# Performance work log

Hardware: AMD Instinct MI355X
Metric: run time of the kernel (lower is better)

## Reference

```python
import jax, jax.numpy as jnp
import numpy as np

TEMPERATURE = 0.07
NORMALIZE = True
NEG_INF = -1e30


def setup_inputs() -> dict:
    key = jax.random.key(0)
    features = jax.random.normal(key, (8192, 512), dtype=jnp.float32)
    return {"features": features}


def reference(features):
    # features: [B, D]
    B = features.shape[0]
    if NORMALIZE:
        norm = jnp.linalg.norm(features, axis=1, keepdims=True)
        features = features / jnp.maximum(norm, 1e-12)
    # [B, B] similarity matrix
    sim = jnp.matmul(features, features.T) / TEMPERATURE

    # default SimCLR labels: arange(B//2) repeated twice -> pair (i, i + B//2)
    half = jnp.arange(B // 2, dtype=jnp.int32)
    labels = jnp.concatenate([half, half])
    eq = labels[None, :] == labels[:, None]          # [B, B]
    diag = jnp.eye(B, dtype=bool)
    mask_pos = eq & ~diag                            # positives per row

    # Original per-row CE: logits = cat(pos_sims, neg_sims) (= all j != i),
    # target index 0 = FIRST positive (lowest column index). Loss_i =
    # logsumexp_{j != i}(sim[i, j]) - sim[i, first_pos_i].
    sim_masked = jnp.where(diag, NEG_INF, sim)
    lse = jax.scipy.special.logsumexp(sim_masked, axis=1)   # [B]

    first_pos = jnp.argmax(mask_pos, axis=1)                 # first True per row
    pos_sim = jnp.take_along_axis(sim, first_pos[:, None], axis=1)[:, 0]

    has_pos = jnp.any(mask_pos, axis=1)
    losses = jnp.where(has_pos, lse - pos_sim, 0.0)
    count = jnp.maximum(jnp.sum(has_pos.astype(jnp.float32)), 1.0)
    return jnp.sum(losses) / count
```

## Files before the change

### kernel.cpp

```cpp
#include <hip/hip_runtime.h>
#include <hip/hip_bf16.h>
#include <stdint.h>

#define BATCH 8192
#define DIM   512
#define TILE  128
#define BK    64
#define NT    (BATCH / TILE)
#define NPAIR (NT * (NT + 1) / 2)
#define NXCD  8

#define FEAT_SCALE 4.5398164f
#define LN2        0.69314718055994531f

typedef __attribute__((ext_vector_type(8))) short short8;
typedef __attribute__((ext_vector_type(4))) float f32x4;

__device__ __forceinline__ void gld_lds16(const void* g, void* l) {
  __builtin_amdgcn_global_load_lds(
      (__attribute__((address_space(1))) void*)(uintptr_t)g,
      (__attribute__((address_space(3))) void*)(uintptr_t)l,
      16, 0, 0);
}

__global__ __launch_bounds__(256) void normalize_bf16(
    const float* __restrict__ x, __hip_bfloat16* __restrict__ o,
    float* __restrict__ rowsum) {
  const int wv = threadIdx.x >> 6, lane = threadIdx.x & 63;
  const int row = blockIdx.x * 4 + wv;
  if (lane == 0) rowsum[row] = 0.0f;
  const float4* xr = (const float4*)(x + (size_t)row * DIM);
  const float4 v0 = xr[lane];
  const float4 v1 = xr[lane + 64];
  float ss = v0.x * v0.x + v0.y * v0.y + v0.z * v0.z + v0.w * v0.w +
             v1.x * v1.x + v1.y * v1.y + v1.z * v1.z + v1.w * v1.w;
#pragma unroll
  for (int m = 32; m > 0; m >>= 1) ss += __shfl_xor(ss, m, 64);
  const float inv = FEAT_SCALE / fmaxf(sqrtf(ss), 1e-12f);
  ushort4 p0, p1;
  p0.x = __bfloat16_as_ushort(__float2bfloat16(v0.x * inv));
  p0.y = __bfloat16_as_ushort(__float2bfloat16(v0.y * inv));
  p0.z = __bfloat16_as_ushort(__float2bfloat16(v0.z * inv));
  p0.w = __bfloat16_as_ushort(__float2bfloat16(v0.w * inv));
  p1.x = __bfloat16_as_ushort(__float2bfloat16(v1.x * inv));
  p1.y = __bfloat16_as_ushort(__float2bfloat16(v1.y * inv));
  p1.z = __bfloat16_as_ushort(__float2bfloat16(v1.z * inv));
  p1.w = __bfloat16_as_ushort(__float2bfloat16(v1.w * inv));
  ushort4* orow = (ushort4*)(o + (size_t)row * DIM);
  orow[lane]      = p0;
  orow[lane + 64] = p1;
}

__global__ __launch_bounds__(256, 4) void sim_lse_kernel(
    const __hip_bfloat16* __restrict__ F, float* __restrict__ rowsum,
    float* __restrict__ possim) {
  __shared__ __hip_bfloat16 smem[2 * TILE * BK];
  __shared__ float rowAcc[TILE];
  __shared__ float colAcc[TILE];

  const int t = (blockIdx.x % NXCD) * (NPAIR / NXCD) + blockIdx.x / NXCD;

  int by = (int)((129.0f - sqrtf(129.0f * 129.0f - 8.0f * (float)t)) * 0.5f);
  if (by > NT - 1) by = NT - 1;
  if (by < 0) by = 0;
  while ((by + 1) * (129 - (by + 1)) / 2 <= t) ++by;
  while (by * (129 - by) / 2 > t) --by;
  const int bx = by + (t - by * (129 - by) / 2);
  const bool diagTile = (bx == by);

  const int rowBase = by * TILE;
  const int colBase = bx * TILE;

  const int tid   = threadIdx.x;
  const int lane  = tid & 63;
  const int wv    = tid >> 6;
  const int waveM = wv >> 1;
  const int waveN = wv & 1;
  const int quad  = lane >> 4;
  const int l15   = lane & 15;

  if (tid < TILE) { rowAcc[tid] = 0.0f; colAcc[tid] = 0.0f; }

  f32x4 acc[4][4] = {};

  const int sb = lane & 7;
  const __hip_bfloat16* gA[4];
  const __hip_bfloat16* gB[4];
  char* ldsA[4];
  char* ldsB[4];
#pragma unroll
  for (int c = 0; c < 4; ++c) {
    const int sRow = wv * 32 + c * 8 + (lane >> 3);
    const int g = sb ^ (sRow & 7);
    gA[c] = F + (size_t)(rowBase + sRow) * DIM + g * 8;
    gB[c] = F + (size_t)(colBase + sRow) * DIM + g * 8;
    ldsA[c] = (char*)smem + (wv * 4 + c) * 1024;
    ldsB[c] = (char*)smem + 16384 + (wv * 4 + c) * 1024;
  }

  int aOff[4], bOff[4];
#pragma unroll
  for (int i = 0; i < 4; ++i) {
    const int Ra = waveM * 64 + i * 16 + l15;
    aOff[i] = Ra * 128 + (quad ^ (Ra & 7)) * 16;
    const int Rb = waveN * 64 + i * 16 + l15;
    bOff[i] = 16384 + Rb * 128 + (quad ^ (Rb & 7)) * 16;
  }
  char* sbase = (char*)smem;

  for (int k0 = 0; k0 < DIM; k0 += BK) {
#pragma unroll
    for (int c = 0; c < 4; ++c) {
      gld_lds16(gA[c] + k0, ldsA[c]);
      gld_lds16(gB[c] + k0, ldsB[c]);
    }
    __syncthreads();

    short8 a[4], b[4];
#pragma unroll
    for (int i = 0; i < 4; ++i) {
      a[i] = *(const short8*)(sbase + aOff[i]);
      b[i] = *(const short8*)(sbase + bOff[i]);
    }
#pragma unroll
    for (int mi = 0; mi < 4; ++mi)
#pragma unroll
      for (int ni = 0; ni < 4; ++ni)
        acc[mi][ni] =
            __builtin_amdgcn_mfma_f32_16x16x32_bf16(a[mi], b[ni], acc[mi][ni], 0, 0, 0);
#pragma unroll
    for (int i = 0; i < 4; ++i) {
      a[i] = *(const short8*)(sbase + (aOff[i] ^ 64));
      b[i] = *(const short8*)(sbase + (bOff[i] ^ 64));
    }
#pragma unroll
    for (int mi = 0; mi < 4; ++mi)
#pragma unroll
      for (int ni = 0; ni < 4; ++ni)
        acc[mi][ni] =
            __builtin_amdgcn_mfma_f32_16x16x32_bf16(a[mi], b[ni], acc[mi][ni], 0, 0, 0);
    __syncthreads();
  }

  if (diagTile) {
#pragma unroll
    for (int mi = 0; mi < 4; ++mi) {
#pragma unroll
      for (int r = 0; r < 4; ++r) {
        const int lrow = waveM * 64 + mi * 16 + quad * 4 + r;
        float rsum = 0.0f;
#pragma unroll
        for (int ni = 0; ni < 4; ++ni) {
          const int lcol = waveN * 64 + ni * 16 + l15;
          rsum += (lcol == lrow) ? 0.0f : exp2f(acc[mi][ni][r]);
        }
#pragma unroll
        for (int m = 1; m < 16; m <<= 1) rsum += __shfl_xor(rsum, m, 64);
        if (l15 == 0) atomicAdd(&rowAcc[lrow], rsum);
      }
    }
  } else {
    const bool hasPos = (bx == by + 32);
    float colpart[4] = {0.0f, 0.0f, 0.0f, 0.0f};
#pragma unroll
    for (int mi = 0; mi < 4; ++mi) {
#pragma unroll
      for (int r = 0; r < 4; ++r) {
        const int lrow = waveM * 64 + mi * 16 + quad * 4 + r;
        float rsum = 0.0f;
#pragma unroll
        for (int ni = 0; ni < 4; ++ni) {
          const float s = acc[mi][ni][r];
          const float e = exp2f(s);
          rsum += e;
          colpart[ni] += e;
          if (hasPos) {
            const int lcol = waveN * 64 + ni * 16 + l15;
            if (lcol == lrow) {
              const int gi = rowBase + lrow;
              possim[gi] = s;
              possim[gi + 4096] = s;
            }
          }
        }
#pragma unroll
        for (int m = 1; m < 16; m <<= 1) rsum += __shfl_xor(rsum, m, 64);
        if (l15 == 0) atomicAdd(&rowAcc[lrow], rsum);
      }
    }
#pragma unroll
    for (int ni = 0; ni < 4; ++ni) {
      float c = colpart[ni];
      c += __shfl_xor(c, 16, 64);
      c += __shfl_xor(c, 32, 64);
      if (quad == 0) atomicAdd(&colAcc[waveN * 64 + ni * 16 + l15], c);
    }
  }
  __syncthreads();
  if (tid < TILE) {
    atomicAdd(&rowsum[rowBase + tid], rowAcc[tid]);
    if (!diagTile) atomicAdd(&rowsum[colBase + tid], colAcc[tid]);
  }
}

__global__ __launch_bounds__(1024) void finalize_kernel(
    const float* __restrict__ rowsum, const float* __restrict__ possim,
    float* __restrict__ out) {
  float acc = 0.0f;
  for (int i = threadIdx.x; i < BATCH; i += 1024)
    acc += __logf(rowsum[i]) - possim[i] * LN2;
#pragma unroll
  for (int m = 32; m > 0; m >>= 1) acc += __shfl_xor(acc, m, 64);
  __shared__ float ws[16];
  const int lane = threadIdx.x & 63, wv = threadIdx.x >> 6;
  if (lane == 0) ws[wv] = acc;
  __syncthreads();
  if (threadIdx.x == 0) {
    float tot = 0.0f;
#pragma unroll
    for (int k = 0; k < 16; ++k) tot += ws[k];
    out[0] = tot * (1.0f / (float)BATCH);
  }
}

extern "C" void kernel_launch(void* const* d_in, const int* in_sizes, int n_in,
                              void* d_out, int out_size, void* d_ws, size_t ws_size,
                              hipStream_t stream) {
  const float* x = (const float*)d_in[0];
  float* out = (float*)d_out;

  __hip_bfloat16* Fb = (__hip_bfloat16*)d_ws;
  float* rowsum = (float*)((char*)d_ws + (size_t)BATCH * DIM * sizeof(__hip_bfloat16));
  float* possim = rowsum + BATCH;

  normalize_bf16<<<BATCH / 4, 256, 0, stream>>>(x, Fb, rowsum);
  sim_lse_kernel<<<NPAIR, 256, 0, stream>>>(Fb, rowsum, possim);
  finalize_kernel<<<1, 1024, 0, stream>>>(rowsum, possim, out);
}
```

Baseline: 130.0 us.

## Replace shuffle+LDS-atomic row reduction with padded LDS transpose; drop XCD swizzle

```diff
diff --git a/kernel.cpp b/kernel.cpp
--- a/kernel.cpp
+++ b/kernel.cpp
@@ -8,7 +8,6 @@
 #define BK    64
 #define NT    (BATCH / TILE)
 #define NPAIR (NT * (NT + 1) / 2)
-#define NXCD  8
 
 #define FEAT_SCALE 4.5398164f
 #define LN2        0.69314718055994531f
@@ -55,11 +54,9 @@
     const __hip_bfloat16* __restrict__ F, float* __restrict__ rowsum,
     float* __restrict__ possim) {
   __shared__ __hip_bfloat16 smem[2 * TILE * BK];
-  __shared__ float rowAcc[TILE];
   __shared__ float colAcc[TILE];
 
-  const int t = (blockIdx.x % NXCD) * (NPAIR / NXCD) + blockIdx.x / NXCD;
-
+  const int t = blockIdx.x;
   int by = (int)((129.0f - sqrtf(129.0f * 129.0f - 8.0f * (float)t)) * 0.5f);
   if (by > NT - 1) by = NT - 1;
   if (by < 0) by = 0;
@@ -79,7 +76,7 @@
   const int quad  = lane >> 4;
   const int l15   = lane & 15;
 
-  if (tid < TILE) { rowAcc[tid] = 0.0f; colAcc[tid] = 0.0f; }
+  if (tid < TILE) colAcc[tid] = 0.0f;
 
   f32x4 acc[4][4] = {};
 
@@ -142,52 +139,53 @@
     __syncthreads();
   }
 
+  float* redBuf = (float*)smem;
+  f32x4 rsumv[4] = {};
+  float colpart[4] = {0.0f, 0.0f, 0.0f, 0.0f};
+
   if (diagTile) {
 #pragma unroll
-    for (int mi = 0; mi < 4; ++mi) {
-#pragma unroll
-      for (int r = 0; r < 4; ++r) {
-        const int lrow = waveM * 64 + mi * 16 + quad * 4 + r;
-        float rsum = 0.0f;
-#pragma unroll
-        for (int ni = 0; ni < 4; ++ni) {
-          const int lcol = waveN * 64 + ni * 16 + l15;
-          rsum += (lcol == lrow) ? 0.0f : exp2f(acc[mi][ni][r]);
+    for (int mi = 0; mi < 4; ++mi)
+#pragma unroll
+      for (int ni = 0; ni < 4; ++ni)
+#pragma unroll
+        for (int r = 0; r < 4; ++r) {
+          const int rl = waveM * 64 + mi * 16 + quad * 4 + r;
+          const int cl = waveN * 64 + ni * 16 + l15;
+          rsumv[mi][r] += (cl == rl) ? 0.0f : exp2f(acc[mi][ni][r]);
         }
-#pragma unroll
-        for (int m = 1; m < 16; m <<= 1) rsum += __shfl_xor(rsum, m, 64);
-        if (l15 == 0) atomicAdd(&rowAcc[lrow], rsum);
-      }
-    }
   } else {
     const bool hasPos = (bx == by + 32);
-    float colpart[4] = {0.0f, 0.0f, 0.0f, 0.0f};
-#pragma unroll
-    for (int mi = 0; mi < 4; ++mi) {
-#pragma unroll
-      for (int r = 0; r < 4; ++r) {
-        const int lrow = waveM * 64 + mi * 16 + quad * 4 + r;
-        float rsum = 0.0f;
-#pragma unroll
-        for (int ni = 0; ni < 4; ++ni) {
+#pragma unroll
+    for (int mi = 0; mi < 4; ++mi)
+#pragma unroll
+      for (int ni = 0; ni < 4; ++ni)
+#pragma unroll
+        for (int r = 0; r < 4; ++r) {
           const float s = acc[mi][ni][r];
           const float e = exp2f(s);
-          rsum += e;
+          rsumv[mi][r] += e;
           colpart[ni] += e;
           if (hasPos) {
-            const int lcol = waveN * 64 + ni * 16 + l15;
-            if (lcol == lrow) {
-              const int gi = rowBase + lrow;
+            const int rl = waveM * 64 + mi * 16 + quad * 4 + r;
+            const int cl = waveN * 64 + ni * 16 + l15;
+            if (cl == rl) {
+              const int gi = rowBase + rl;
               possim[gi] = s;
               possim[gi + 4096] = s;
             }
           }
         }
-#pragma unroll
-        for (int m = 1; m < 16; m <<= 1) rsum += __shfl_xor(rsum, m, 64);
-        if (l15 == 0) atomicAdd(&rowAcc[lrow], rsum);
-      }
-    }
+  }
+
+  {
+    float* wbase = redBuf + ((waveN * 2 + waveM) * 16 + l15) * 68 + quad * 4;
+#pragma unroll
+    for (int mi = 0; mi < 4; ++mi)
+      *(f32x4*)(wbase + mi * 16) = rsumv[mi];
+  }
+
+  if (!diagTile) {
 #pragma unroll
     for (int ni = 0; ni < 4; ++ni) {
       float c = colpart[ni];
@@ -197,10 +195,18 @@
     }
   }
   __syncthreads();
-  if (tid < TILE) {
-    atomicAdd(&rowsum[rowBase + tid], rowAcc[tid]);
-    if (!diagTile) atomicAdd(&rowsum[colBase + tid], colAcc[tid]);
-  }
+
+  {
+    const int wn = tid >> 7, r = tid & 127;
+    const int strip = r >> 6, rl = r & 63;
+    const float* base = redBuf + ((wn * 2 + strip) * 16) * 68 + rl;
+    float s = 0.0f;
+#pragma unroll
+    for (int j = 0; j < 16; ++j) s += base[j * 68];
+    atomicAdd(&rowsum[rowBase + r], s);
+  }
+  if (tid < TILE && !diagTile)
+    atomicAdd(&rowsum[colBase + tid], colAcc[tid]);
 }
 
 __global__ __launch_bounds__(1024) void finalize_kernel(
```

After: 111.7 us. -14.1%, faster.
